# Optimization experiments

Measured on AMD Instinct MI355X. Metric: run time of the kernel, lower is better.

The kernel has to match this reference:

```python
import jax, jax.numpy as jnp
import numpy as np

N_NODES = 50000
N_EDGES = 500000
HIDDEN = 64
NUM_BASIS = 32
NUM_SH = 4  # (lmax+1)^2 with lmax=1


def _mlp(x, w1, b1, w2, b2):
    # Linear -> SiLU -> Linear, matching nn.Sequential(Linear, SiLU, Linear)
    return jax.nn.silu(x @ w1 + b1) @ w2 + b2


def setup_inputs() -> dict:
    key = jax.random.key(0)
    ks = jax.random.split(key, 10)
    scale_in = 1.0 / np.sqrt(NUM_BASIS)
    scale_h = 1.0 / np.sqrt(HIDDEN)
    return {
        "scalar": jax.random.normal(ks[0], (N_NODES, HIDDEN), dtype=jnp.float32),
        "vector": jax.random.normal(ks[1], (N_NODES, 3, HIDDEN), dtype=jnp.float32),
        "edge_sh": jax.random.normal(ks[2], (N_EDGES, NUM_SH), dtype=jnp.float32),
        "edge_length": jax.random.uniform(ks[3], (N_EDGES, NUM_BASIS), dtype=jnp.float32),
        "edge_index": jax.random.randint(ks[4], (2, N_EDGES), 0, N_NODES, dtype=jnp.int32),
        "sw1": jax.random.normal(ks[5], (NUM_BASIS, HIDDEN), dtype=jnp.float32) * scale_in,
        "sb1": jnp.zeros((HIDDEN,), dtype=jnp.float32),
        "sw2": jax.random.normal(ks[6], (HIDDEN, HIDDEN), dtype=jnp.float32) * scale_h,
        "sb2": jnp.zeros((HIDDEN,), dtype=jnp.float32),
        "vw1": jax.random.normal(ks[7], (NUM_BASIS, HIDDEN), dtype=jnp.float32) * scale_in,
        "vb1": jnp.zeros((HIDDEN,), dtype=jnp.float32),
        "vw2": jax.random.normal(ks[8], (HIDDEN, HIDDEN), dtype=jnp.float32) * scale_h,
        "vb2": jnp.zeros((HIDDEN,), dtype=jnp.float32),
    }


def reference(scalar, vector, edge_sh, edge_length, edge_index,
              sw1, sb1, sw2, sb2, vw1, vb1, vw2, vb2):
    # edge_sh is accepted (as in the torch forward signature) but unused.
    row, col = edge_index[0], edge_index[1]
    n = scalar.shape[0]

    # Edge-wise MLP weights from radial basis expansion: [E, hidden]
    scalar_weights = _mlp(edge_length, sw1, sb1, sw2, sb2)
    # Gather source-node scalars, weight, scatter-add to destination nodes.
    scalar_msg = scalar[col] * scalar_weights                   # [E, hidden]
    out_scalar = jax.ops.segment_sum(scalar_msg, row, num_segments=n)

    vector_weights = _mlp(edge_length, vw1, vb1, vw2, vb2)      # [E, hidden]
    vector_msg = vector[col] * vector_weights[:, None, :]       # [E, 3, hidden]
    out_vector = jax.ops.segment_sum(vector_msg, row, num_segments=n)

    return out_scalar, out_vector
```

## Files before the change

### kernel.cpp

```cpp
#include <hip/hip_runtime.h>

#define HIDDEN 64
#define NB 32
#define SCAN_BLOCK 1024
#define HSTR 72

typedef __attribute__((ext_vector_type(8))) short bf16x8;
typedef __attribute__((ext_vector_type(4))) float f32x4;

static __device__ __forceinline__ unsigned short f2bf(float x) {
    union { float f; unsigned u; } v; v.f = x;
    unsigned r = v.u + 0x7fffu + ((v.u >> 16) & 1u);
    return (unsigned short)(r >> 16);
}
static __device__ __forceinline__ float bf2f(unsigned short s) {
    union { unsigned u; float f; } v; v.u = ((unsigned)s) << 16;
    return v.f;
}

__global__ __launch_bounds__(256) void featpack_kernel(
    const float* __restrict__ scalar,
    const float* __restrict__ vector,
    const int*   __restrict__ edge_index,
    int* __restrict__ counts,
    ushort4* __restrict__ feat,
    int total, int E, int do_feat)
{
    int i = blockIdx.x * 256 + threadIdx.x;
    if (i < E) atomicAdd(&counts[edge_index[i]], 1);
    if (!do_feat || i >= total) return;
    const int n = i >> 6, l = i & 63;
    const float* vp = vector + (size_t)n * 192 + l;
    ushort4 o;
    o.x = f2bf(scalar[i]);
    o.y = f2bf(vp[0]);
    o.z = f2bf(vp[64]);
    o.w = f2bf(vp[128]);
    feat[i] = o;
}

__global__ __launch_bounds__(SCAN_BLOCK) void scan_pass1(
    const int* __restrict__ counts, int* __restrict__ partial,
    int* __restrict__ blocksums, int N)
{
    __shared__ int tmp[SCAN_BLOCK];
    const int t = threadIdx.x;
    const int gid = blockIdx.x * SCAN_BLOCK + t;
    int v = (gid < N) ? counts[gid] : 0;
    tmp[t] = v;
    __syncthreads();
    for (int off = 1; off < SCAN_BLOCK; off <<= 1) {
        int x = (t >= off) ? tmp[t - off] : 0;
        __syncthreads();
        tmp[t] += x;
        __syncthreads();
    }
    if (gid < N) partial[gid] = tmp[t] - v;
    if (t == SCAN_BLOCK - 1) blocksums[blockIdx.x] = tmp[t];
}

__global__ __launch_bounds__(64) void scan_pass2(int* __restrict__ blocksums, int nb)
{
    const int t = threadIdx.x;
    int v = (t < nb) ? blocksums[t] : 0;
    int s = v;
    #pragma unroll
    for (int off = 1; off < 64; off <<= 1) {
        int x = __shfl_up(s, off, 64);
        if (t >= off) s += x;
    }
    if (t < nb) blocksums[t] = s - v;
}

__global__ __launch_bounds__(SCAN_BLOCK) void scan_pass3(
    const int* __restrict__ partial, const int* __restrict__ blocksums,
    int* __restrict__ offsets, int* __restrict__ cursors, int N, int E)
{
    const int gid = blockIdx.x * SCAN_BLOCK + threadIdx.x;
    if (gid < N) {
        int o = partial[gid] + blocksums[blockIdx.x];
        offsets[gid] = o;
        cursors[gid] = o;
    }
    if (blockIdx.x == 0 && threadIdx.x == 0) offsets[N] = E;
}

__global__ __launch_bounds__(256) void scatter_kernel(
    const int* __restrict__ edge_index, int* __restrict__ cursors,
    int* __restrict__ cols, int* __restrict__ eperm, int E)
{
    int i = blockIdx.x * 256 + threadIdx.x;
    if (i < E) {
        int p = atomicAdd(&cursors[edge_index[i]], 1);
        cols[p] = edge_index[E + i];
        eperm[p] = i;
    }
}

__global__ __launch_bounds__(256) void mlp_mfma_kernel(
    const float* __restrict__ edge_length,
    const int*   __restrict__ eperm,
    const float* __restrict__ sw1, const float* __restrict__ sb1,
    const float* __restrict__ sw2, const float* __restrict__ sb2,
    const float* __restrict__ vw1, const float* __restrict__ vb1,
    const float* __restrict__ vw2, const float* __restrict__ vb2,
    unsigned short* __restrict__ W,
    int E, int nchunks)
{
    __shared__ short Hs[4][64 * HSTR];

    const int t    = threadIdx.x;
    const int lane = t & 63;
    const int wid  = t >> 6;
    const int quad = lane >> 4;
    const int l16  = lane & 15;
    short* Hw = Hs[wid];

    const float* w1p[2] = {sw1, vw1};
    const float* b1p[2] = {sb1, vb1};
    const float* w2p[2] = {sw2, vw2};
    const float* b2p[2] = {sb2, vb2};

    bf16x8 w1f[2][4];
    bf16x8 w2f[2][2][4];
    float  b1v[2][4], b2v[2][4];
    #pragma unroll
    for (int m = 0; m < 2; ++m) {
        #pragma unroll
        for (int nt = 0; nt < 4; ++nt) {
            const int col = nt * 16 + l16;
            #pragma unroll
            for (int j = 0; j < 8; ++j)
                w1f[m][nt][j] = (short)f2bf(w1p[m][(quad * 8 + j) * HIDDEN + col]);
            #pragma unroll
            for (int kk = 0; kk < 2; ++kk) {
                #pragma unroll
                for (int j = 0; j < 8; ++j)
                    w2f[m][kk][nt][j] = (short)f2bf(w2p[m][(kk * 32 + quad * 8 + j) * HIDDEN + col]);
            }
            b1v[m][nt] = b1p[m][col];
            b2v[m][nt] = b2p[m][col];
        }
    }

    const int wave_g = blockIdx.x * 4 + wid;
    const int nwaves = gridDim.x * 4;

    for (int c = wave_g; c < nchunks; c += nwaves) {
        const int j0 = c * 64;

        bf16x8 af[4];
        #pragma unroll
        for (int mt = 0; mt < 4; ++mt) {
            int p = j0 + mt * 16 + l16;
            if (p >= E) p = E - 1;
            const int e = eperm[p];
            const float* r = edge_length + (size_t)e * NB + quad * 8;
            float4 u0 = *(const float4*)r;
            float4 u1 = *(const float4*)(r + 4);
            af[mt][0] = (short)f2bf(u0.x); af[mt][1] = (short)f2bf(u0.y);
            af[mt][2] = (short)f2bf(u0.z); af[mt][3] = (short)f2bf(u0.w);
            af[mt][4] = (short)f2bf(u1.x); af[mt][5] = (short)f2bf(u1.y);
            af[mt][6] = (short)f2bf(u1.z); af[mt][7] = (short)f2bf(u1.w);
        }

        #pragma unroll
        for (int m = 0; m < 2; ++m) {
            #pragma unroll
            for (int mt = 0; mt < 4; ++mt) {
                #pragma unroll
                for (int nt = 0; nt < 4; ++nt) {
                    f32x4 cf = {b1v[m][nt], b1v[m][nt], b1v[m][nt], b1v[m][nt]};
                    cf = __builtin_amdgcn_mfma_f32_16x16x32_bf16(af[mt], w1f[m][nt], cf, 0, 0, 0);
                    #pragma unroll
                    for (int r4 = 0; r4 < 4; ++r4) {
                        float x = cf[r4];
                        x = x * __builtin_amdgcn_rcpf(1.0f + __expf(-x));
                        const int row = mt * 16 + quad * 4 + r4;
                        Hw[row * HSTR + nt * 16 + l16] = (short)f2bf(x);
                    }
                }
            }

            #pragma unroll
            for (int mt = 0; mt < 4; ++mt) {
                const int arow = mt * 16 + l16;
                bf16x8 a0 = *(const bf16x8*)(Hw + arow * HSTR + quad * 8);
                bf16x8 a1 = *(const bf16x8*)(Hw + arow * HSTR + 32 + quad * 8);
                #pragma unroll
                for (int nt = 0; nt < 4; ++nt) {
                    f32x4 cf = {b2v[m][nt], b2v[m][nt], b2v[m][nt], b2v[m][nt]};
                    cf = __builtin_amdgcn_mfma_f32_16x16x32_bf16(a1, w2f[m][1][nt], cf, 0, 0, 0);
                    cf = __builtin_amdgcn_mfma_f32_16x16x32_bf16(a0, w2f[m][0][nt], cf, 0, 0, 0);
                    #pragma unroll
                    for (int r4 = 0; r4 < 4; ++r4) {
                        const int row = mt * 16 + quad * 4 + r4;
                        Hw[row * HSTR + nt * 16 + l16] = (short)f2bf(cf[r4]);
                    }
                }
            }

            #pragma unroll
            for (int i = 0; i < 8; ++i) {
                const int row = i * 8 + (lane >> 3);
                bf16x8 v = *(const bf16x8*)(Hw + row * HSTR + (lane & 7) * 8);
                if (j0 + row < E)
                    *(bf16x8*)(W + (size_t)(j0 + row) * 128 + m * 64 + (lane & 7) * 8) = v;
            }
        }
    }
}

__global__ __launch_bounds__(256) void node_kernel_feat(
    const ushort4* __restrict__ feat,
    const int* __restrict__ offsets,
    const int* __restrict__ cols,
    const unsigned short* __restrict__ W,
    float* __restrict__ out_scalar,
    float* __restrict__ out_vector,
    int N)
{
    const int lane = threadIdx.x & 63;
    const int wave = blockIdx.x * 4 + (threadIdx.x >> 6);
    const int nw   = gridDim.x * 4;

    for (int n = wave; n < N; n += nw) {
        const int beg = offsets[n];
        const int end = offsets[n + 1];

        float as = 0.0f, a0 = 0.0f, a1 = 0.0f, a2 = 0.0f;

        for (int base = beg; base < end; base += 64) {
            const int cnt = (end - base < 64) ? (end - base) : 64;

            int mycol = 0;
            if (lane < cnt) mycol = cols[base + lane];

            const int c0 = __shfl(mycol, 0, 64);
            const unsigned short* wp0 = W + (size_t)base * 128;
            float ws = bf2f(wp0[lane]);
            float wv = bf2f(wp0[64 + lane]);
            ushort4 f = feat[(size_t)c0 * 64 + lane];

            for (int k = 0; k < cnt; ++k) {
                const int kn = (k + 1 < cnt) ? k + 1 : k;
                const int cn = __shfl(mycol, kn, 64);
                const unsigned short* wpn = W + (size_t)(base + kn) * 128;
                const float wsn = bf2f(wpn[lane]);
                const float wvn = bf2f(wpn[64 + lane]);
                const ushort4 fn = feat[(size_t)cn * 64 + lane];

                as = fmaf(bf2f(f.x), ws, as);
                a0 = fmaf(bf2f(f.y), wv, a0);
                a1 = fmaf(bf2f(f.z), wv, a1);
                a2 = fmaf(bf2f(f.w), wv, a2);

                ws = wsn; wv = wvn; f = fn;
            }
        }

        out_scalar[(size_t)n * HIDDEN + lane] = as;
        float* ov = out_vector + (size_t)n * 3 * HIDDEN;
        ov[lane]       = a0;
        ov[64 + lane]  = a1;
        ov[128 + lane] = a2;
    }
}

__global__ __launch_bounds__(256) void node_kernel_f32(
    const float* __restrict__ scalar,
    const float* __restrict__ vector,
    const int* __restrict__ offsets,
    const int* __restrict__ cols,
    const unsigned short* __restrict__ W,
    float* __restrict__ out_scalar,
    float* __restrict__ out_vector,
    int N)
{
    const int lane = threadIdx.x & 63;
    const int wave = blockIdx.x * 4 + (threadIdx.x >> 6);
    const int nw   = gridDim.x * 4;

    for (int n = wave; n < N; n += nw) {
        const int beg = offsets[n];
        const int end = offsets[n + 1];
        float as = 0.0f, a0 = 0.0f, a1 = 0.0f, a2 = 0.0f;
        for (int j = beg; j < end; ++j) {
            const unsigned short* wp = W + (size_t)j * 128;
            const float w_s = bf2f(wp[lane]);
            const float w_v = bf2f(wp[64 + lane]);
            const int c = cols[j];
            const float* sp = scalar + (size_t)c * HIDDEN;
            const float* vp = vector + (size_t)c * 3 * HIDDEN;
            as = fmaf(sp[lane],       w_s, as);
            a0 = fmaf(vp[lane],       w_v, a0);
            a1 = fmaf(vp[64 + lane],  w_v, a1);
            a2 = fmaf(vp[128 + lane], w_v, a2);
        }
        out_scalar[(size_t)n * HIDDEN + lane] = as;
        float* ov = out_vector + (size_t)n * 3 * HIDDEN;
        ov[lane]       = a0;
        ov[64 + lane]  = a1;
        ov[128 + lane] = a2;
    }
}

extern "C" void kernel_launch(void* const* d_in, const int* in_sizes, int n_in,
                              void* d_out, int out_size, void* d_ws, size_t ws_size,
                              hipStream_t stream) {
    const float* scalar      = (const float*)d_in[0];
    const float* vector      = (const float*)d_in[1];
    const float* edge_length = (const float*)d_in[3];
    const int*   edge_index  = (const int*)d_in[4];
    const float* sw1 = (const float*)d_in[5];
    const float* sb1 = (const float*)d_in[6];
    const float* sw2 = (const float*)d_in[7];
    const float* sb2 = (const float*)d_in[8];
    const float* vw1 = (const float*)d_in[9];
    const float* vb1 = (const float*)d_in[10];
    const float* vw2 = (const float*)d_in[11];
    const float* vb2 = (const float*)d_in[12];

    const int N = in_sizes[0] / HIDDEN;
    const int E = in_sizes[4] / 2;

    float* out_scalar = (float*)d_out;
    float* out_vector = (float*)d_out + (size_t)N * HIDDEN;

    size_t off = 0;
    unsigned short* W = (unsigned short*)d_ws;
    off += (size_t)E * 128 * 2;
    int* cols = (int*)((char*)d_ws + off);
    off += (size_t)E * 4;
    int* eperm = (int*)((char*)d_ws + off);
    off += (size_t)E * 4;
    int* ib = (int*)((char*)d_ws + off);
    int* counts    = ib;
    int* partial   = ib + N;
    int* offsets   = ib + 2 * N;
    int* cursors   = ib + 3 * N + 1;
    int* blocksums = ib + 4 * N + 1;
    off += ((size_t)4 * N + 1 + 64) * 4;
    off = (off + 15) & ~(size_t)15;
    ushort4* feat = (ushort4*)((char*)d_ws + off);
    const bool use_feat = (off + (size_t)N * 64 * 8) <= ws_size;

    hipMemsetAsync(counts, 0, (size_t)N * sizeof(int), stream);

    const int egrid = (E + 255) / 256;

    {
        const int total = N * 64;
        int cover = total > E ? total : E;
        featpack_kernel<<<(cover + 255) / 256, 256, 0, stream>>>(
            scalar, vector, edge_index, counts, feat, total, E, use_feat ? 1 : 0);
    }

    const int nb = (N + SCAN_BLOCK - 1) / SCAN_BLOCK;
    scan_pass1<<<nb, SCAN_BLOCK, 0, stream>>>(counts, partial, blocksums, N);
    scan_pass2<<<1, 64, 0, stream>>>(blocksums, nb);
    scan_pass3<<<nb, SCAN_BLOCK, 0, stream>>>(partial, blocksums, offsets, cursors, N, E);
    scatter_kernel<<<egrid, 256, 0, stream>>>(edge_index, cursors, cols, eperm, E);

    const int nchunks = (E + 63) / 64;
    mlp_mfma_kernel<<<1024, 256, 0, stream>>>(
        edge_length, eperm,
        sw1, sb1, sw2, sb2, vw1, vb1, vw2, vb2,
        W, E, nchunks);

    const int ngrid = (N + 3) / 4;
    if (use_feat) {
        node_kernel_feat<<<ngrid, 256, 0, stream>>>(
            feat, offsets, cols, W, out_scalar, out_vector, N);
    } else {
        node_kernel_f32<<<ngrid, 256, 0, stream>>>(
            scalar, vector, offsets, cols, W, out_scalar, out_vector, N);
    }
}
```

Before: 343.1 us.

## Fuse edge MLP with segmented atomic aggregation, dropping the W buffer

The per-edge MLP kernel now does the aggregation itself. It walks its 64-edge chunk of row-sorted edges, builds segmented sums straight from the LDS-resident weights, and flushes each row segment to the output with float atomicAdd. This removes the large bf16 edge-weight buffer W, which used to be written to global memory and read back, along with the separate node-gather kernel. The outputs are now zeroed inside featpack, and the fp32 fallback path is removed. In exchange it adds global atomics at every segment boundary and on rows that span chunks, makes summation order nondeterministic, and assumes the workspace always fits the packed feature buffer.

```diff
diff --git a/kernel.cpp b/kernel.cpp
--- a/kernel.cpp
+++ b/kernel.cpp
@@ -24,11 +24,14 @@
     const int*   __restrict__ edge_index,
     int* __restrict__ counts,
     ushort4* __restrict__ feat,
-    int total, int E, int do_feat)
+    float4* __restrict__ out_zero,
+    int total, int E)
 {
     int i = blockIdx.x * 256 + threadIdx.x;
     if (i < E) atomicAdd(&counts[edge_index[i]], 1);
-    if (!do_feat || i >= total) return;
+    if (i >= total) return;
+    const float4 z = {0.f, 0.f, 0.f, 0.f};
+    out_zero[i] = z;
     const int n = i >> 6, l = i & 63;
     const float* vp = vector + (size_t)n * 192 + l;
     ushort4 o;
@@ -87,24 +90,31 @@
 
 __global__ __launch_bounds__(256) void scatter_kernel(
     const int* __restrict__ edge_index, int* __restrict__ cursors,
-    int* __restrict__ cols, int* __restrict__ eperm, int E)
+    int* __restrict__ cols, int* __restrict__ rows,
+    int* __restrict__ eperm, int E)
 {
     int i = blockIdx.x * 256 + threadIdx.x;
     if (i < E) {
-        int p = atomicAdd(&cursors[edge_index[i]], 1);
+        const int r = edge_index[i];
+        int p = atomicAdd(&cursors[r], 1);
         cols[p] = edge_index[E + i];
+        rows[p] = r;
         eperm[p] = i;
     }
 }
 
-__global__ __launch_bounds__(256) void mlp_mfma_kernel(
+__global__ __launch_bounds__(256) void fused_kernel(
     const float* __restrict__ edge_length,
     const int*   __restrict__ eperm,
+    const int*   __restrict__ cols,
+    const int*   __restrict__ rows,
+    const ushort4* __restrict__ feat,
     const float* __restrict__ sw1, const float* __restrict__ sb1,
     const float* __restrict__ sw2, const float* __restrict__ sb2,
     const float* __restrict__ vw1, const float* __restrict__ vb1,
     const float* __restrict__ vw2, const float* __restrict__ vb2,
-    unsigned short* __restrict__ W,
+    float* __restrict__ out_scalar,
+    float* __restrict__ out_vector,
     int E, int nchunks)
 {
     __shared__ short Hs[4][64 * HSTR];
@@ -147,7 +157,14 @@
     const int nwaves = gridDim.x * 4;
 
     for (int c = wave_g; c < nchunks; c += nwaves) {
-        const int j0 = c * 64;
+        const int j0  = c * 64;
+        const int cnt = (E - j0 < 64) ? (E - j0) : 64;
+
+        int mycol = 0, myrow = 0;
+        if (lane < cnt) {
+            mycol = cols[j0 + lane];
+            myrow = rows[j0 + lane];
+        }
 
         bf16x8 af[4];
         #pragma unroll
@@ -200,108 +217,53 @@
                 }
             }
 
-            #pragma unroll
-            for (int i = 0; i < 8; ++i) {
-                const int row = i * 8 + (lane >> 3);
-                bf16x8 v = *(const bf16x8*)(Hw + row * HSTR + (lane & 7) * 8);
-                if (j0 + row < E)
-                    *(bf16x8*)(W + (size_t)(j0 + row) * 128 + m * 64 + (lane & 7) * 8) = v;
+            if (m == 0) {
+                int node_cur = __shfl(myrow, 0, 64);
+                const int c0 = __shfl(mycol, 0, 64);
+                float wcur = bf2f((unsigned short)Hw[lane]);
+                ushort4 f = feat[(size_t)c0 * 64 + lane];
+                float acc = 0.f;
+                for (int k = 0; k < cnt; ++k) {
+                    const int kn = (k + 1 < cnt) ? k + 1 : k;
+                    const float wn = bf2f((unsigned short)Hw[kn * HSTR + lane]);
+                    const int cn = __shfl(mycol, kn, 64);
+                    const ushort4 fn = feat[(size_t)cn * 64 + lane];
+                    const int node_n = (k + 1 < cnt) ? __shfl(myrow, kn, 64) : -1;
+                    acc = fmaf(bf2f(f.x), wcur, acc);
+                    if (node_n != node_cur) {
+                        atomicAdd(out_scalar + (size_t)node_cur * HIDDEN + lane, acc);
+                        acc = 0.f;
+                        node_cur = node_n;
+                    }
+                    wcur = wn; f = fn;
+                }
+            } else {
+                int node_cur = __shfl(myrow, 0, 64);
+                const int c0 = __shfl(mycol, 0, 64);
+                float wcur = bf2f((unsigned short)Hw[lane]);
+                ushort4 f = feat[(size_t)c0 * 64 + lane];
+                float a0 = 0.f, a1 = 0.f, a2 = 0.f;
+                for (int k = 0; k < cnt; ++k) {
+                    const int kn = (k + 1 < cnt) ? k + 1 : k;
+                    const float wn = bf2f((unsigned short)Hw[kn * HSTR + lane]);
+                    const int cn = __shfl(mycol, kn, 64);
+                    const ushort4 fn = feat[(size_t)cn * 64 + lane];
+                    const int node_n = (k + 1 < cnt) ? __shfl(myrow, kn, 64) : -1;
+                    a0 = fmaf(bf2f(f.y), wcur, a0);
+                    a1 = fmaf(bf2f(f.z), wcur, a1);
+                    a2 = fmaf(bf2f(f.w), wcur, a2);
+                    if (node_n != node_cur) {
+                        float* ov = out_vector + (size_t)node_cur * 192;
+                        atomicAdd(ov + lane,        a0);
+                        atomicAdd(ov + 64 + lane,   a1);
+                        atomicAdd(ov + 128 + lane,  a2);
+                        a0 = 0.f; a1 = 0.f; a2 = 0.f;
+                        node_cur = node_n;
+                    }
+                    wcur = wn; f = fn;
+                }
             }
         }
-    }
-}
-
-__global__ __launch_bounds__(256) void node_kernel_feat(
-    const ushort4* __restrict__ feat,
-    const int* __restrict__ offsets,
-    const int* __restrict__ cols,
-    const unsigned short* __restrict__ W,
-    float* __restrict__ out_scalar,
-    float* __restrict__ out_vector,
-    int N)
-{
-    const int lane = threadIdx.x & 63;
-    const int wave = blockIdx.x * 4 + (threadIdx.x >> 6);
-    const int nw   = gridDim.x * 4;
-
-    for (int n = wave; n < N; n += nw) {
-        const int beg = offsets[n];
-        const int end = offsets[n + 1];
-
-        float as = 0.0f, a0 = 0.0f, a1 = 0.0f, a2 = 0.0f;
-
-        for (int base = beg; base < end; base += 64) {
-            const int cnt = (end - base < 64) ? (end - base) : 64;
-
-            int mycol = 0;
-            if (lane < cnt) mycol = cols[base + lane];
-
-            const int c0 = __shfl(mycol, 0, 64);
-            const unsigned short* wp0 = W + (size_t)base * 128;
-            float ws = bf2f(wp0[lane]);
-            float wv = bf2f(wp0[64 + lane]);
-            ushort4 f = feat[(size_t)c0 * 64 + lane];
-
-            for (int k = 0; k < cnt; ++k) {
-                const int kn = (k + 1 < cnt) ? k + 1 : k;
-                const int cn = __shfl(mycol, kn, 64);
-                const unsigned short* wpn = W + (size_t)(base + kn) * 128;
-                const float wsn = bf2f(wpn[lane]);
-                const float wvn = bf2f(wpn[64 + lane]);
-                const ushort4 fn = feat[(size_t)cn * 64 + lane];
-
-                as = fmaf(bf2f(f.x), ws, as);
-                a0 = fmaf(bf2f(f.y), wv, a0);
-                a1 = fmaf(bf2f(f.z), wv, a1);
-                a2 = fmaf(bf2f(f.w), wv, a2);
-
-                ws = wsn; wv = wvn; f = fn;
-            }
-        }
-
-        out_scalar[(size_t)n * HIDDEN + lane] = as;
-        float* ov = out_vector + (size_t)n * 3 * HIDDEN;
-        ov[lane]       = a0;
-        ov[64 + lane]  = a1;
-        ov[128 + lane] = a2;
-    }
-}
-
-__global__ __launch_bounds__(256) void node_kernel_f32(
-    const float* __restrict__ scalar,
-    const float* __restrict__ vector,
-    const int* __restrict__ offsets,
-    const int* __restrict__ cols,
-    const unsigned short* __restrict__ W,
-    float* __restrict__ out_scalar,
-    float* __restrict__ out_vector,
-    int N)
-{
-    const int lane = threadIdx.x & 63;
-    const int wave = blockIdx.x * 4 + (threadIdx.x >> 6);
-    const int nw   = gridDim.x * 4;
-
-    for (int n = wave; n < N; n += nw) {
-        const int beg = offsets[n];
-        const int end = offsets[n + 1];
-        float as = 0.0f, a0 = 0.0f, a1 = 0.0f, a2 = 0.0f;
-        for (int j = beg; j < end; ++j) {
-            const unsigned short* wp = W + (size_t)j * 128;
-            const float w_s = bf2f(wp[lane]);
-            const float w_v = bf2f(wp[64 + lane]);
-            const int c = cols[j];
-            const float* sp = scalar + (size_t)c * HIDDEN;
-            const float* vp = vector + (size_t)c * 3 * HIDDEN;
-            as = fmaf(sp[lane],       w_s, as);
-            a0 = fmaf(vp[lane],       w_v, a0);
-            a1 = fmaf(vp[64 + lane],  w_v, a1);
-            a2 = fmaf(vp[128 + lane], w_v, a2);
-        }
-        out_scalar[(size_t)n * HIDDEN + lane] = as;
-        float* ov = out_vector + (size_t)n * 3 * HIDDEN;
-        ov[lane]       = a0;
-        ov[64 + lane]  = a1;
-        ov[128 + lane] = a2;
     }
 }
 
@@ -328,9 +290,9 @@
     float* out_vector = (float*)d_out + (size_t)N * HIDDEN;
 
     size_t off = 0;
-    unsigned short* W = (unsigned short*)d_ws;
-    off += (size_t)E * 128 * 2;
     int* cols = (int*)((char*)d_ws + off);
+    off += (size_t)E * 4;
+    int* rows = (int*)((char*)d_ws + off);
     off += (size_t)E * 4;
     int* eperm = (int*)((char*)d_ws + off);
     off += (size_t)E * 4;
@@ -343,37 +305,24 @@
     off += ((size_t)4 * N + 1 + 64) * 4;
     off = (off + 15) & ~(size_t)15;
     ushort4* feat = (ushort4*)((char*)d_ws + off);
-    const bool use_feat = (off + (size_t)N * 64 * 8) <= ws_size;
 
     hipMemsetAsync(counts, 0, (size_t)N * sizeof(int), stream);
 
     const int egrid = (E + 255) / 256;
-
-    {
-        const int total = N * 64;
-        int cover = total > E ? total : E;
-        featpack_kernel<<<(cover + 255) / 256, 256, 0, stream>>>(
-            scalar, vector, edge_index, counts, feat, total, E, use_feat ? 1 : 0);
-    }
+    const int total = N * 64;
+
+    featpack_kernel<<<(total + 255) / 256, 256, 0, stream>>>(
+        scalar, vector, edge_index, counts, feat, (float4*)d_out, total, E);
 
     const int nb = (N + SCAN_BLOCK - 1) / SCAN_BLOCK;
     scan_pass1<<<nb, SCAN_BLOCK, 0, stream>>>(counts, partial, blocksums, N);
     scan_pass2<<<1, 64, 0, stream>>>(blocksums, nb);
     scan_pass3<<<nb, SCAN_BLOCK, 0, stream>>>(partial, blocksums, offsets, cursors, N, E);
-    scatter_kernel<<<egrid, 256, 0, stream>>>(edge_index, cursors, cols, eperm, E);
+    scatter_kernel<<<egrid, 256, 0, stream>>>(edge_index, cursors, cols, rows, eperm, E);
 
     const int nchunks = (E + 63) / 64;
-    mlp_mfma_kernel<<<1024, 256, 0, stream>>>(
-        edge_length, eperm,
+    fused_kernel<<<1024, 256, 0, stream>>>(
+        edge_length, eperm, cols, rows, feat,
         sw1, sb1, sw2, sb2, vw1, vb1, vw2, vb2,
-        W, E, nchunks);
-
-    const int ngrid = (N + 3) / 4;
-    if (use_feat) {
-        node_kernel_feat<<<ngrid, 256, 0, stream>>>(
-            feat, offsets, cols, W, out_scalar, out_vector, N);
-    } else {
-        node_kernel_f32<<<ngrid, 256, 0, stream>>>(
-            scalar, vector, offsets, cols, W, out_scalar, out_vector, N);
-    }
-}
+        out_scalar, out_vector, E, nchunks);
+}
```

After: 466.7 us. +36.0%, slower.

## Fuse scan and scatter into one cooperative kernel; vectorize feature packing

Applied to the files above, without the earlier changes.

The three-pass prefix scan and the edge scatter are merged into a single cooperative kernel that uses grid-wide syncs, with a fixed grid of 256 blocks of 512 threads. This removes several small kernel launches and the intermediate partial-sum buffer. The featpack kernel now processes two elements per thread, using float2 loads and 16-byte bf16 stores, and counts two edges per thread. The fixed cooperative grid only covers up to 131072 nodes, and grid.sync adds its own synchronization cost.

```diff
diff --git a/kernel.cpp b/kernel.cpp
--- a/kernel.cpp
+++ b/kernel.cpp
@@ -1,12 +1,17 @@
 #include <hip/hip_runtime.h>
+#include <hip/hip_cooperative_groups.h>
+
+namespace cg = cooperative_groups;
 
 #define HIDDEN 64
 #define NB 32
-#define SCAN_BLOCK 1024
 #define HSTR 72
+#define CS_THREADS 512
+#define CS_BLOCKS 256
 
 typedef __attribute__((ext_vector_type(8))) short bf16x8;
 typedef __attribute__((ext_vector_type(4))) float f32x4;
+typedef __attribute__((ext_vector_type(8))) unsigned short u16x8;
 
 static __device__ __forceinline__ unsigned short f2bf(float x) {
     union { float f; unsigned u; } v; v.f = x;
@@ -23,75 +28,80 @@
     const float* __restrict__ vector,
     const int*   __restrict__ edge_index,
     int* __restrict__ counts,
-    ushort4* __restrict__ feat,
+    u16x8* __restrict__ featv,
     int total, int E, int do_feat)
 {
-    int i = blockIdx.x * 256 + threadIdx.x;
-    if (i < E) atomicAdd(&counts[edge_index[i]], 1);
-    if (!do_feat || i >= total) return;
-    const int n = i >> 6, l = i & 63;
+    const int idx   = blockIdx.x * 256 + threadIdx.x;
+    const int base2 = idx * 2;
+    if (base2 < E)     atomicAdd(&counts[edge_index[base2]], 1);
+    if (base2 + 1 < E) atomicAdd(&counts[edge_index[base2 + 1]], 1);
+    if (!do_feat || base2 >= total) return;
+    const int n = base2 >> 6, l = base2 & 63;
     const float* vp = vector + (size_t)n * 192 + l;
-    ushort4 o;
-    o.x = f2bf(scalar[i]);
-    o.y = f2bf(vp[0]);
-    o.z = f2bf(vp[64]);
-    o.w = f2bf(vp[128]);
-    feat[i] = o;
-}
-
-__global__ __launch_bounds__(SCAN_BLOCK) void scan_pass1(
-    const int* __restrict__ counts, int* __restrict__ partial,
-    int* __restrict__ blocksums, int N)
-{
-    __shared__ int tmp[SCAN_BLOCK];
-    const int t = threadIdx.x;
-    const int gid = blockIdx.x * SCAN_BLOCK + t;
+    const float2 s2 = *(const float2*)(scalar + base2);
+    const float2 w0 = *(const float2*)(vp);
+    const float2 w1 = *(const float2*)(vp + 64);
+    const float2 w2 = *(const float2*)(vp + 128);
+    u16x8 o;
+    o[0] = f2bf(s2.x); o[1] = f2bf(w0.x); o[2] = f2bf(w1.x); o[3] = f2bf(w2.x);
+    o[4] = f2bf(s2.y); o[5] = f2bf(w0.y); o[6] = f2bf(w1.y); o[7] = f2bf(w2.y);
+    featv[idx] = o;
+}
+
+__global__ __launch_bounds__(CS_THREADS) void scan_scatter_kernel(
+    const int* __restrict__ edge_index,
+    const int* __restrict__ counts,
+    int* __restrict__ offsets,
+    int* __restrict__ cursors,
+    int* __restrict__ blocksums,
+    int* __restrict__ cols,
+    int* __restrict__ eperm,
+    int N, int E)
+{
+    cg::grid_group grid = cg::this_grid();
+    __shared__ int tmp[CS_THREADS];
+    const int t   = threadIdx.x;
+    const int gid = blockIdx.x * CS_THREADS + t;
+
     int v = (gid < N) ? counts[gid] : 0;
     tmp[t] = v;
     __syncthreads();
-    for (int off = 1; off < SCAN_BLOCK; off <<= 1) {
+    for (int off = 1; off < CS_THREADS; off <<= 1) {
         int x = (t >= off) ? tmp[t - off] : 0;
         __syncthreads();
         tmp[t] += x;
         __syncthreads();
     }
-    if (gid < N) partial[gid] = tmp[t] - v;
-    if (t == SCAN_BLOCK - 1) blocksums[blockIdx.x] = tmp[t];
-}
-
-__global__ __launch_bounds__(64) void scan_pass2(int* __restrict__ blocksums, int nb)
-{
-    const int t = threadIdx.x;
-    int v = (t < nb) ? blocksums[t] : 0;
-    int s = v;
-    #pragma unroll
-    for (int off = 1; off < 64; off <<= 1) {
-        int x = __shfl_up(s, off, 64);
-        if (t >= off) s += x;
-    }
-    if (t < nb) blocksums[t] = s - v;
-}
-
-__global__ __launch_bounds__(SCAN_BLOCK) void scan_pass3(
-    const int* __restrict__ partial, const int* __restrict__ blocksums,
-    int* __restrict__ offsets, int* __restrict__ cursors, int N, int E)
-{
-    const int gid = blockIdx.x * SCAN_BLOCK + threadIdx.x;
+    const int excl = tmp[t] - v;
+    if (t == CS_THREADS - 1) blocksums[blockIdx.x] = tmp[t];
+    grid.sync();
+
+    if (blockIdx.x == 0) {
+        int b = (t < CS_BLOCKS) ? blocksums[t] : 0;
+        tmp[t] = b;
+        __syncthreads();
+        for (int off = 1; off < CS_THREADS; off <<= 1) {
+            int x = (t >= off) ? tmp[t - off] : 0;
+            __syncthreads();
+            tmp[t] += x;
+            __syncthreads();
+        }
+        if (t < CS_BLOCKS) blocksums[t] = tmp[t] - b;
+    }
+    grid.sync();
+
     if (gid < N) {
-        int o = partial[gid] + blocksums[blockIdx.x];
+        const int o = excl + blocksums[blockIdx.x];
         offsets[gid] = o;
         cursors[gid] = o;
     }
-    if (blockIdx.x == 0 && threadIdx.x == 0) offsets[N] = E;
-}
-
-__global__ __launch_bounds__(256) void scatter_kernel(
-    const int* __restrict__ edge_index, int* __restrict__ cursors,
-    int* __restrict__ cols, int* __restrict__ eperm, int E)
-{
-    int i = blockIdx.x * 256 + threadIdx.x;
-    if (i < E) {
-        int p = atomicAdd(&cursors[edge_index[i]], 1);
+    if (gid == N) offsets[N] = E;
+    grid.sync();
+
+    const int nth = CS_BLOCKS * CS_THREADS;
+    for (int i = gid; i < E; i += nth) {
+        const int r = edge_index[i];
+        int p = atomicAdd(&cursors[r], 1);
         cols[p] = edge_index[E + i];
         eperm[p] = i;
     }
@@ -336,31 +346,35 @@
     off += (size_t)E * 4;
     int* ib = (int*)((char*)d_ws + off);
     int* counts    = ib;
-    int* partial   = ib + N;
-    int* offsets   = ib + 2 * N;
-    int* cursors   = ib + 3 * N + 1;
-    int* blocksums = ib + 4 * N + 1;
-    off += ((size_t)4 * N + 1 + 64) * 4;
+    int* offsets   = ib + N;
+    int* cursors   = ib + 2 * N + 1;
+    int* blocksums = ib + 3 * N + 1;
+    off += ((size_t)3 * N + 1 + CS_BLOCKS) * 4;
     off = (off + 15) & ~(size_t)15;
     ushort4* feat = (ushort4*)((char*)d_ws + off);
     const bool use_feat = (off + (size_t)N * 64 * 8) <= ws_size;
 
     hipMemsetAsync(counts, 0, (size_t)N * sizeof(int), stream);
 
-    const int egrid = (E + 255) / 256;
+    const int total = N * 64;
 
     {
-        const int total = N * 64;
-        int cover = total > E ? total : E;
-        featpack_kernel<<<(cover + 255) / 256, 256, 0, stream>>>(
-            scalar, vector, edge_index, counts, feat, total, E, use_feat ? 1 : 0);
-    }
-
-    const int nb = (N + SCAN_BLOCK - 1) / SCAN_BLOCK;
-    scan_pass1<<<nb, SCAN_BLOCK, 0, stream>>>(counts, partial, blocksums, N);
-    scan_pass2<<<1, 64, 0, stream>>>(blocksums, nb);
-    scan_pass3<<<nb, SCAN_BLOCK, 0, stream>>>(partial, blocksums, offsets, cursors, N, E);
-    scatter_kernel<<<egrid, 256, 0, stream>>>(edge_index, cursors, cols, eperm, E);
+        const int nthreads = total / 2;
+        featpack_kernel<<<(nthreads + 255) / 256, 256, 0, stream>>>(
+            scalar, vector, edge_index, counts, (u16x8*)feat,
+            total, E, use_feat ? 1 : 0);
+    }
+
+    {
+        void* args[] = {
+            (void*)&edge_index, (void*)&counts, (void*)&offsets,
+            (void*)&cursors, (void*)&blocksums, (void*)&cols, (void*)&eperm,
+            (void*)&N, (void*)&E
+        };
+        hipLaunchCooperativeKernel((void*)scan_scatter_kernel,
+                                   dim3(CS_BLOCKS), dim3(CS_THREADS),
+                                   args, 0, stream);
+    }
 
     const int nchunks = (E + 63) / 64;
     mlp_mfma_kernel<<<1024, 256, 0, stream>>>(
```

New measurement: 433.4 us. +26.3%, slower.
